# Kernel optimization log

Hardware: AMD Instinct MI355X
Metric: run time of the kernel (lower is better)

The kernel has to match this reference:

```python
import math
import jax, jax.numpy as jnp
import numpy as np

D_MODEL = 1024
N_HEAD = 16
HEAD_DIM = D_MODEL // N_HEAD


def _alibi_slopes(n_heads: int) -> np.ndarray:
    def pow2_slopes(n):
        start = 2.0 ** (-(2.0 ** (-(math.log2(n) - 3))))
        return [start * (start ** i) for i in range(n)]
    if math.log2(n_heads).is_integer():
        slopes = pow2_slopes(n_heads)
    else:
        cp2 = 2 ** math.floor(math.log2(n_heads))
        slopes = pow2_slopes(cp2)
        slopes += pow2_slopes(2 * cp2)[0::2][: n_heads - cp2]
    return np.asarray(slopes, dtype=np.float32)


def setup_inputs() -> dict:
    key = jax.random.key(0)
    ks = jax.random.split(key, 12)
    B, N, D = 2, 2048, D_MODEL
    s = 1.0 / math.sqrt(D)
    inp = {
        "x_q": jax.random.normal(ks[0], (B, N, D), dtype=jnp.float32),
        "x_kv": jax.random.normal(ks[1], (B, N, D), dtype=jnp.float32),
        "attn_bias": jax.random.normal(ks[2], (N, N), dtype=jnp.float32) * 0.1,
        "Wq": jax.random.normal(ks[3], (D, D), dtype=jnp.float32) * s,
        "bq": jnp.zeros((D,), dtype=jnp.float32),
        "Wk": jax.random.normal(ks[4], (D, D), dtype=jnp.float32) * s,
        "bk": jnp.zeros((D,), dtype=jnp.float32),
        "Wv": jax.random.normal(ks[5], (D, D), dtype=jnp.float32) * s,
        "bv": jnp.zeros((D,), dtype=jnp.float32),
        "Wo": jax.random.normal(ks[6], (D, D), dtype=jnp.float32) * s,
        "bo": jnp.zeros((D,), dtype=jnp.float32),
        "is_self_attn": 1,
        "causal": 1,
    }
    return inp


def reference(x_q, x_kv, attn_bias, Wq, bq, Wk, bk, Wv, bv, Wo, bo, is_self_attn, causal):
    B, Nq, D = x_q.shape
    Nk = x_kv.shape[1]
    H, hd = N_HEAD, HEAD_DIM

    # torch Linear: y = x @ W.T + b
    q = (jnp.einsum("bqd,ed->bqe", x_q, Wq) + bq).reshape(B, Nq, H, hd)
    k = (jnp.einsum("bkd,ed->bke", x_kv, Wk) + bk).reshape(B, Nk, H, hd)
    v = (jnp.einsum("bkd,ed->bke", x_kv, Wv) + bv).reshape(B, Nk, H, hd)

    logits = jnp.einsum("bqhd,bkhd->bhqk", q, k) / math.sqrt(hd)  # [B,H,Nq,Nk]

    if is_self_attn and Nq == Nk:
        i = jnp.arange(Nq)[:, None]
        j = jnp.arange(Nk)[None, :]
        dist = jnp.maximum(j - i, 0).astype(jnp.float32)  # [Nq,Nk]
        slopes = jnp.asarray(_alibi_slopes(H))  # [H]
        logits = logits - slopes[None, :, None, None] * dist[None, None]

    if attn_bias is not None:
        logits = logits + attn_bias[None, None]

    if causal and is_self_attn and Nq == Nk:
        mask = jnp.triu(jnp.ones((Nq, Nk), dtype=bool), k=1)
        logits = jnp.where(mask[None, None], -jnp.inf, logits)

    attn = jax.nn.softmax(logits, axis=-1)
    out = jnp.einsum("bhqk,bkhd->bqhd", attn, v).reshape(B, Nq, D)
    return jnp.einsum("bqd,ed->bqe", out, Wo) + bo
```

## Files before the change

### kernel.cpp

```cpp
#include <hip/hip_runtime.h>
#include <hip/hip_bf16.h>

typedef __attribute__((ext_vector_type(8))) short short8;
typedef __attribute__((ext_vector_type(4))) float floatx4;

#define NSEQ   2048
#define DMODEL 1024
#define NHEAD  16
#define HDIM   64
#define BATCH  2
#define LOG2E 1.44269504088896340736f

#define XF4   1048576u
#define WF4   262144u

__device__ __forceinline__ void gload16(const void* g, void* l) {
    __builtin_amdgcn_global_load_lds(
        (const __attribute__((address_space(1))) void*)g,
        (__attribute__((address_space(3))) void*)l, 16, 0, 0);
}

#define BARRIER() asm volatile("s_barrier" ::: "memory")
#define CFENCE()  asm volatile("" ::: "memory")

__device__ __forceinline__ float bf16lo(unsigned u) {
    union { unsigned i; float f; } c; c.i = u << 16; return c.f;
}
__device__ __forceinline__ float bf16hi(unsigned u) {
    union { unsigned i; float f; } c; c.i = u & 0xffff0000u; return c.f;
}

__global__ __launch_bounds__(256)
void cvt_all(const float* __restrict__ xq, const float* __restrict__ xkv,
             const float* __restrict__ wq, const float* __restrict__ wk,
             const float* __restrict__ wv, const float* __restrict__ wo,
             __hip_bfloat16* __restrict__ dxq, __hip_bfloat16* __restrict__ dxkv,
             __hip_bfloat16* __restrict__ dwq, __hip_bfloat16* __restrict__ dwk,
             __hip_bfloat16* __restrict__ dwv, __hip_bfloat16* __restrict__ dwo)
{
    const unsigned total = 2*XF4 + 4*WF4;
    const unsigned stride = gridDim.x * blockDim.x;
    for (unsigned i = blockIdx.x*blockDim.x + threadIdx.x; i < total; i += stride) {
        const float4* src; __hip_bfloat16* dst; unsigned off;
        if (i < XF4)        { src = (const float4*)xq;  dst = dxq;  off = i; }
        else if (i < 2*XF4) { src = (const float4*)xkv; dst = dxkv; off = i - XF4; }
        else {
            unsigned j = i - 2*XF4; unsigned ws = j >> 18; off = j & (WF4 - 1);
            src = (const float4*)(ws==0 ? wq : ws==1 ? wk : ws==2 ? wv : wo);
            dst = (ws==0 ? dwq : ws==1 ? dwk : ws==2 ? dwv : dwo);
        }
        float4 v = src[off];
        __hip_bfloat16 h[4] = {__float2bfloat16(v.x), __float2bfloat16(v.y),
                               __float2bfloat16(v.z), __float2bfloat16(v.w)};
        *reinterpret_cast<uint2*>(dst + (size_t)off*4) = *reinterpret_cast<uint2*>(h);
    }
}

__global__ __launch_bounds__(256)
void cvt_bias(const float* __restrict__ src, __hip_bfloat16* __restrict__ dst)
{
    const unsigned total = (unsigned)(NSEQ*(size_t)NSEQ/4);
    const unsigned stride = gridDim.x * blockDim.x;
    for (unsigned i = blockIdx.x*blockDim.x + threadIdx.x; i < total; i += stride) {
        float4 v = ((const float4*)src)[i];
        __hip_bfloat16 h[4] = {__float2bfloat16(v.x * LOG2E), __float2bfloat16(v.y * LOG2E),
                               __float2bfloat16(v.z * LOG2E), __float2bfloat16(v.w * LOG2E)};
        *reinterpret_cast<uint2*>(dst + (size_t)i*4) = *reinterpret_cast<uint2*>(h);
    }
}

struct QkvArgs {
    const __hip_bfloat16* A[3];
    const __hip_bfloat16* W[3];
    const float*          bias[3];
    __hip_bfloat16*       out[3];
};

__global__ __launch_bounds__(256)
void qkv_gemm(QkvArgs args)
{
    __shared__ __hip_bfloat16 S[256][72];

    const int tid  = threadIdx.x;
    const int lane = tid & 63;
    const int wv   = tid >> 6;
    const int wm   = wv >> 1, wn = wv & 1;
    const int l15  = lane & 15, l4 = lane >> 4;
    const int m0   = blockIdx.x * 128;
    const int n0   = blockIdx.y * 128;
    const int z    = blockIdx.z;

    const __hip_bfloat16* __restrict__ A = args.A[z];
    const __hip_bfloat16* __restrict__ W = args.W[z];

    floatx4 acc[4][4] = {};

    for (int k0 = 0; k0 < DMODEL; k0 += 64) {
        #pragma unroll
        for (int it = 0; it < 4; ++it) {
            const int sI   = tid + 256 * it;
            const int row  = sI >> 2;
            const int colq = (sI & 3) * 16;
            const __hip_bfloat16* src = (it < 2)
                ? A + (size_t)(m0 + row) * DMODEL + k0 + colq
                : W + (size_t)(n0 + row - 128) * DMODEL + k0 + colq;
            const uint4* s4 = reinterpret_cast<const uint4*>(src);
            *reinterpret_cast<uint4*>(&S[row][colq])     = s4[0];
            *reinterpret_cast<uint4*>(&S[row][colq + 8]) = s4[1];
        }
        __syncthreads();

        #pragma unroll
        for (int kk = 0; kk < 64; kk += 32) {
            short8 af[4], bf[4];
            #pragma unroll
            for (int mi = 0; mi < 4; ++mi)
                af[mi] = *reinterpret_cast<const short8*>(&S[wm*64 + mi*16 + l15][kk + l4*8]);
            #pragma unroll
            for (int nj = 0; nj < 4; ++nj)
                bf[nj] = *reinterpret_cast<const short8*>(&S[128 + wn*64 + nj*16 + l15][kk + l4*8]);
            #pragma unroll
            for (int mi = 0; mi < 4; ++mi)
                #pragma unroll
                for (int nj = 0; nj < 4; ++nj)
                    acc[mi][nj] = __builtin_amdgcn_mfma_f32_16x16x32_bf16(
                        af[mi], bf[nj], acc[mi][nj], 0, 0, 0);
        }
        __syncthreads();
    }

    const float* bias = args.bias[z];
    __hip_bfloat16* C = args.out[z];
    const bool vt = (z == 2);
    #pragma unroll
    for (int mi = 0; mi < 4; ++mi) {
        const int mbase = m0 + wm*64 + mi*16 + l4*4;
        #pragma unroll
        for (int nj = 0; nj < 4; ++nj) {
            const int nn = n0 + wn*64 + nj*16 + l15;
            const float bb = bias[nn];
            const int h = nn >> 6, d = nn & (HDIM - 1);
            #pragma unroll
            for (int r = 0; r < 4; ++r) {
                const int m = mbase + r;
                const int b = m >> 11, n = m & (NSEQ - 1);
                const float val = acc[mi][nj][r] + bb;
                if (!vt)
                    C[((size_t)(b*NHEAD + h) * NSEQ + n) * HDIM + d] = __float2bfloat16(val);
                else
                    C[((size_t)(b*NHEAD + h) * HDIM + d) * NSEQ + n] = __float2bfloat16(val);
            }
        }
    }
}

__global__ __launch_bounds__(256)
void oproj_gemm(const __hip_bfloat16* __restrict__ A, const __hip_bfloat16* __restrict__ W,
                const float* __restrict__ bias, float* __restrict__ C)
{
    __shared__ __hip_bfloat16 S[192][72];

    const int tid  = threadIdx.x;
    const int lane = tid & 63;
    const int wv   = tid >> 6;
    const int l15  = lane & 15, l4 = lane >> 4;
    const int m0   = blockIdx.x * 64;
    const int n0   = blockIdx.y * 128;

    floatx4 acc[4][2] = {};

    for (int k0 = 0; k0 < DMODEL; k0 += 64) {
        #pragma unroll
        for (int it = 0; it < 3; ++it) {
            const int sI   = tid + 256 * it;
            const int row  = sI >> 2;
            const int colq = (sI & 3) * 16;
            const __hip_bfloat16* src = (it < 1)
                ? A + (size_t)(m0 + row) * DMODEL + k0 + colq
                : W + (size_t)(n0 + row - 64) * DMODEL + k0 + colq;
            const uint4* s4 = reinterpret_cast<const uint4*>(src);
            *reinterpret_cast<uint4*>(&S[row][colq])     = s4[0];
            *reinterpret_cast<uint4*>(&S[row][colq + 8]) = s4[1];
        }
        __syncthreads();

        #pragma unroll
        for (int kk = 0; kk < 64; kk += 32) {
            short8 af[4], bf[2];
            #pragma unroll
            for (int mi = 0; mi < 4; ++mi)
                af[mi] = *reinterpret_cast<const short8*>(&S[mi*16 + l15][kk + l4*8]);
            #pragma unroll
            for (int nj = 0; nj < 2; ++nj)
                bf[nj] = *reinterpret_cast<const short8*>(&S[64 + wv*32 + nj*16 + l15][kk + l4*8]);
            #pragma unroll
            for (int mi = 0; mi < 4; ++mi)
                #pragma unroll
                for (int nj = 0; nj < 2; ++nj)
                    acc[mi][nj] = __builtin_amdgcn_mfma_f32_16x16x32_bf16(
                        af[mi], bf[nj], acc[mi][nj], 0, 0, 0);
        }
        __syncthreads();
    }

    #pragma unroll
    for (int mi = 0; mi < 4; ++mi) {
        const int mbase = m0 + mi*16 + l4*4;
        #pragma unroll
        for (int nj = 0; nj < 2; ++nj) {
            const int nn = n0 + wv*32 + nj*16 + l15;
            const float bb = bias[nn];
            #pragma unroll
            for (int r = 0; r < 4; ++r)
                C[(size_t)(mbase + r) * DMODEL + nn] = acc[mi][nj][r] + bb;
        }
    }
}

__global__ __launch_bounds__(256)
void flash_attn(const __hip_bfloat16* __restrict__ Q,
                const __hip_bfloat16* __restrict__ K,
                const __hip_bfloat16* __restrict__ VT,
                const __hip_bfloat16* __restrict__ Bb,
                const int* __restrict__ selfp,
                const int* __restrict__ causalp,
                __hip_bfloat16* __restrict__ Oout)
{
    __shared__ __align__(16) char KB[2][8192];
    __shared__ __align__(16) char VB[2][8192];
    __shared__ __align__(16) char BBUF[2][8192];
    __shared__ __align__(16) char PL[4][2048];

    const int tid  = threadIdx.x;
    const int lane = tid & 63;
    const int wv   = tid >> 6;
    const int l15  = lane & 15, l4 = lane >> 4;

    const int g   = blockIdx.x;
    const int bh  = g & 31;
    const int u   = g >> 5;
    const int qA  = u, qB = 31 - u;
    const int h   = bh & (NHEAD - 1);
    const int b   = bh >> 4;

    const int selfF   = selfp[0];
    const int causalF = causalp[0];
    const bool cz      = (selfF != 0) && (causalF != 0);
    const bool alibiOn = (selfF != 0) && (causalF == 0);
    const float slopeL2 = exp2f(-(8.0f / NHEAD) * (float)(h + 1)) * LOG2E;

    const char* Kh = (const char*)(K  + (size_t)bh * NSEQ * HDIM);
    const char* Vh = (const char*)(VT + (size_t)bh * HDIM * NSEQ);
    const __hip_bfloat16* Qh = Q + (size_t)bh * NSEQ * HDIM;

    const int nA = cz ? (qA + 1) : (NSEQ/64);
    const int NT = cz ? 33 : (NSEQ/32);

    const int qa0 = qA*64 + wv*16, qb0 = qB*64 + wv*16;
    const short8 qfA0 = *(const short8*)&Qh[(qa0 + l15)*HDIM + l4*8];
    const short8 qfA1 = *(const short8*)&Qh[(qa0 + l15)*HDIM + 32 + l4*8];
    const short8 qfB0 = *(const short8*)&Qh[(qb0 + l15)*HDIM + l4*8];
    const short8 qfB1 = *(const short8*)&Qh[(qb0 + l15)*HDIM + 32 + l4*8];
    CFENCE();

    const int srow = lane >> 3;
    const int co   = (((lane & 7) ^ srow) << 4);

    auto stage = [&](int it_, int bi) {
        int qq, jt;
        if (it_ < nA) { qq = qA; jt = it_; } else { qq = qB; jt = it_ - nA; }
        const int j0 = jt << 6;
        const char* Bh = (const char*)Bb + (size_t)qq * 64 * (NSEQ*2);
        #pragma unroll
        for (int i2 = 0; i2 < 2; ++i2) {
            const int rl = wv*16 + i2*8 + srow;
            const int db = (wv*16 + i2*8) * 128;
            gload16(Kh + (size_t)(j0 + rl)*128 + co,          &KB[bi][db]);
            gload16(Vh + (size_t)rl*4096 + (size_t)j0*2 + co, &VB[bi][db]);
            gload16(Bh + (size_t)rl*4096 + (size_t)j0*2 + co, &BBUF[bi][db]);
        }
    };

    char* plw = &PL[wv][l15 * 128];
    const int swq = (l15 & 7) << 4;
    const int rowb = wv*16 + l15;
    const int swb  = (rowb & 7) << 4;

    floatx4 o[4] = {};
    float lr = 0.f;
    short8 qf0 = qfA0, qf1 = qfA1;
    int qbc = qA;

    stage(0, 0);
    int cur = 0;
    for (int it = 0; it < NT; ++it) {
        if (it + 1 < NT) {
            stage(it + 1, cur ^ 1);
            asm volatile("s_waitcnt vmcnt(6)" ::: "memory");
        } else {
            asm volatile("s_waitcnt vmcnt(0)" ::: "memory");
        }
        BARRIER();

        const char* kb = KB[cur];
        const char* vb = VB[cur];
        const char* bb = BBUF[cur];

        floatx4 s4[4];
        __builtin_amdgcn_s_setprio(1);
        #pragma unroll
        for (int tt = 0; tt < 4; ++tt) {
            const int row = tt*16 + l15;
            const int sw  = (row & 7) << 4;
            const short8 kf0 = *(const short8*)(kb + ((row*128 + l4*16)      ^ sw));
            const short8 kf1 = *(const short8*)(kb + ((row*128 + 64 + l4*16) ^ sw));
            floatx4 z = {};
            z      = __builtin_amdgcn_mfma_f32_16x16x32_bf16(kf0, qf0, z, 0, 0, 0);
            s4[tt] = __builtin_amdgcn_mfma_f32_16x16x32_bf16(kf1, qf1, z, 0, 0, 0);
        }
        __builtin_amdgcn_s_setprio(0);

        uint2 bl[4];
        #pragma unroll
        for (int tt = 0; tt < 4; ++tt)
            bl[tt] = *(const uint2*)(bb + ((rowb*128 + tt*32 + l4*8) ^ swb));

        const bool domask = cz && (it == nA - 1 || it == NT - 1);
        const int qloc = wv*16 + l15;
        #pragma unroll
        for (int tt = 0; tt < 4; ++tt) {
            float bf[4];
            bf[0] = bf16lo(bl[tt].x); bf[1] = bf16hi(bl[tt].x);
            bf[2] = bf16lo(bl[tt].y); bf[3] = bf16hi(bl[tt].y);
            float e[4];
            #pragma unroll
            for (int r = 0; r < 4; ++r) {
                const int jloc = tt*16 + l4*4 + r;
                float v2 = fmaf(s4[tt][r], 0.125f * LOG2E, bf[r]);
                if (alibiOn) {
                    const int jg = ((it < nA) ? it : it - nA)*64 + jloc;
                    const int dd = jg - (qbc*64 + qloc);
                    if (dd > 0) v2 = fmaf((float)dd, -slopeL2, v2);
                }
                e[r] = __builtin_amdgcn_exp2f(v2);
                if (domask && jloc > qloc) e[r] = 0.0f;
                lr += e[r];
            }
            unsigned p0, p1;
            asm("v_cvt_pk_bf16_f32 %0, %1, %2" : "=v"(p0) : "v"(e[0]), "v"(e[1]));
            asm("v_cvt_pk_bf16_f32 %0, %1, %2" : "=v"(p1) : "v"(e[2]), "v"(e[3]));
            uint2 pw; pw.x = p0; pw.y = p1;
            *(uint2*)(plw + ((tt*32 + l4*8) ^ swq)) = pw;
        }

        const short8 pf0 = *(const short8*)(plw + ((l4*16)      ^ swq));
        const short8 pf1 = *(const short8*)(plw + ((64 + l4*16) ^ swq));

        __builtin_amdgcn_s_setprio(1);
        #pragma unroll
        for (int dt = 0; dt < 4; ++dt) {
            const int row = dt*16 + l15;
            const int sw  = (row & 7) << 4;
            const short8 vf0 = *(const short8*)(vb + ((row*128 + l4*16)      ^ sw));
            const short8 vf1 = *(const short8*)(vb + ((row*128 + 64 + l4*16) ^ sw));
            o[dt] = __builtin_amdgcn_mfma_f32_16x16x32_bf16(pf0, vf0, o[dt], 0, 0, 0);
            o[dt] = __builtin_amdgcn_mfma_f32_16x16x32_bf16(pf1, vf1, o[dt], 0, 0, 0);
        }
        __builtin_amdgcn_s_setprio(0);

        BARRIER();
        cur ^= 1;

        if (it == nA - 1 || it == NT - 1) {
            float t = lr;
            t += __shfl_xor(t, 16);
            t += __shfl_xor(t, 32);
            #pragma unroll
            for (int r = 0; r < 4; ++r) {
                const float lq  = __shfl(t, l4*4 + r);
                const float inv = 1.0f / lq;
                const int n = qbc*64 + wv*16 + l4*4 + r;
                #pragma unroll
                for (int dt = 0; dt < 4; ++dt)
                    Oout[((size_t)(b*NSEQ + n)) * DMODEL + h*HDIM + dt*16 + l15] =
                        __float2bfloat16(o[dt][r] * inv);
            }
            if (it == nA - 1) {
                #pragma unroll
                for (int dt = 0; dt < 4; ++dt) o[dt] = floatx4{0.f, 0.f, 0.f, 0.f};
                lr = 0.f;
                qf0 = qfB0; qf1 = qfB1; qbc = qB;
            }
        }
    }
}

extern "C" void kernel_launch(void* const* d_in, const int* in_sizes, int n_in,
                              void* d_out, int out_size, void* d_ws, size_t ws_size,
                              hipStream_t stream)
{
    (void)in_sizes; (void)n_in; (void)out_size; (void)ws_size;
    const float* x_q  = (const float*)d_in[0];
    const float* x_kv = (const float*)d_in[1];
    const float* ab   = (const float*)d_in[2];
    const float* Wq   = (const float*)d_in[3];
    const float* bq   = (const float*)d_in[4];
    const float* Wk   = (const float*)d_in[5];
    const float* bk   = (const float*)d_in[6];
    const float* Wv   = (const float*)d_in[7];
    const float* bv   = (const float*)d_in[8];
    const float* Wo   = (const float*)d_in[9];
    const float* bo   = (const float*)d_in[10];
    const int* selfp   = (const int*)d_in[11];
    const int* causalp = (const int*)d_in[12];

    const size_t XB = (size_t)BATCH * NSEQ * DMODEL * sizeof(__hip_bfloat16);
    const size_t WB = (size_t)DMODEL * DMODEL * sizeof(__hip_bfloat16);
    char* ws = (char*)d_ws;
    __hip_bfloat16* xq_b  = (__hip_bfloat16*)(ws);
    __hip_bfloat16* AO    = (__hip_bfloat16*)(ws);
    __hip_bfloat16* xkv_b = (__hip_bfloat16*)(ws + XB);
    __hip_bfloat16* ab_b  = (__hip_bfloat16*)(ws + XB);
    __hip_bfloat16* Wq_b  = (__hip_bfloat16*)(ws + 2*XB);
    __hip_bfloat16* Wk_b  = (__hip_bfloat16*)(ws + 2*XB + WB);
    __hip_bfloat16* Wv_b  = (__hip_bfloat16*)(ws + 2*XB + 2*WB);
    __hip_bfloat16* Wo_b  = (__hip_bfloat16*)(ws + 2*XB + 3*WB);
    __hip_bfloat16* Qb    = (__hip_bfloat16*)(ws + 2*XB + 4*WB);
    __hip_bfloat16* Kb    = (__hip_bfloat16*)(ws + 2*XB + 4*WB + XB);
    __hip_bfloat16* VTb   = (__hip_bfloat16*)(ws + 2*XB + 4*WB + 2*XB);

    cvt_all<<<dim3(2048), dim3(256), 0, stream>>>(
        x_q, x_kv, Wq, Wk, Wv, Wo, xq_b, xkv_b, Wq_b, Wk_b, Wv_b, Wo_b);

    QkvArgs qa;
    qa.A[0] = xq_b;  qa.A[1] = xkv_b; qa.A[2] = xkv_b;
    qa.W[0] = Wq_b;  qa.W[1] = Wk_b;  qa.W[2] = Wv_b;
    qa.bias[0] = bq; qa.bias[1] = bk; qa.bias[2] = bv;
    qa.out[0] = Qb;  qa.out[1] = Kb;  qa.out[2] = VTb;
    qkv_gemm<<<dim3(32, 8, 3), dim3(256), 0, stream>>>(qa);

    cvt_bias<<<dim3(1024), dim3(256), 0, stream>>>(ab, ab_b);

    flash_attn<<<dim3(512), dim3(256), 0, stream>>>(
        Qb, Kb, VTb, ab_b, selfp, causalp, AO);

    oproj_gemm<<<dim3(64, 8), dim3(256), 0, stream>>>(AO, Wo_b, bo, (float*)d_out);
}
```

Before: 132.9 us.

## Split flash attention query tile and key range across waves, double grid

The flash attention kernel now launches twice as many blocks, each handling half of a 64-row query tile. The four waves are arranged as two query groups times two key halves, and the partial outputs and row sums are merged through shared memory at the end of each tile. V fragments are now loaded directly from global memory into registers rather than staged in LDS, which shrinks LDS use and allows a 4-blocks-per-CU launch bound. The aim is more occupancy and parallelism, at the cost of duplicated K loads per block, extra barriers for the merge, and uncached-through-LDS V reads.

```diff
diff --git a/kernel.cpp b/kernel.cpp
--- a/kernel.cpp
+++ b/kernel.cpp
@@ -217,7 +217,7 @@
     }
 }
 
-__global__ __launch_bounds__(256)
+__global__ __launch_bounds__(256, 4)
 void flash_attn(const __hip_bfloat16* __restrict__ Q,
                 const __hip_bfloat16* __restrict__ K,
                 const __hip_bfloat16* __restrict__ VT,
@@ -227,18 +227,23 @@
                 __hip_bfloat16* __restrict__ Oout)
 {
     __shared__ __align__(16) char KB[2][8192];
-    __shared__ __align__(16) char VB[2][8192];
-    __shared__ __align__(16) char BBUF[2][8192];
-    __shared__ __align__(16) char PL[4][2048];
+    __shared__ __align__(16) char BBUF[2][4096];
+    __shared__ __hip_bfloat16 PL[4][16][40];
+    __shared__ float OX[2][16][68];
+    __shared__ float LR[2][16];
 
     const int tid  = threadIdx.x;
     const int lane = tid & 63;
     const int wv   = tid >> 6;
     const int l15  = lane & 15, l4 = lane >> 4;
+    const int qg   = wv >> 1;
+    const int jh   = wv & 1;
 
     const int g   = blockIdx.x;
     const int bh  = g & 31;
-    const int u   = g >> 5;
+    const int rem = g >> 5;
+    const int u   = rem & 15;
+    const int rh  = rem >> 4;
     const int qA  = u, qB = 31 - u;
     const int h   = bh & (NHEAD - 1);
     const int b   = bh >> 4;
@@ -254,13 +259,14 @@
     const __hip_bfloat16* Qh = Q + (size_t)bh * NSEQ * HDIM;
 
     const int nA = cz ? (qA + 1) : (NSEQ/64);
-    const int NT = cz ? 33 : (NSEQ/32);
-
-    const int qa0 = qA*64 + wv*16, qb0 = qB*64 + wv*16;
-    const short8 qfA0 = *(const short8*)&Qh[(qa0 + l15)*HDIM + l4*8];
-    const short8 qfA1 = *(const short8*)&Qh[(qa0 + l15)*HDIM + 32 + l4*8];
-    const short8 qfB0 = *(const short8*)&Qh[(qb0 + l15)*HDIM + l4*8];
-    const short8 qfB1 = *(const short8*)&Qh[(qb0 + l15)*HDIM + 32 + l4*8];
+    const int NT = cz ? 33 : (2*NSEQ/64);
+
+    const int qloc = rh*32 + qg*16 + l15;
+
+    const short8 qfA0 = *(const short8*)&Qh[(qA*64 + qloc)*HDIM + l4*8];
+    const short8 qfA1 = *(const short8*)&Qh[(qA*64 + qloc)*HDIM + 32 + l4*8];
+    const short8 qfB0 = *(const short8*)&Qh[(qB*64 + qloc)*HDIM + l4*8];
+    const short8 qfB1 = *(const short8*)&Qh[(qB*64 + qloc)*HDIM + 32 + l4*8];
     CFENCE();
 
     const int srow = lane >> 3;
@@ -270,47 +276,51 @@
         int qq, jt;
         if (it_ < nA) { qq = qA; jt = it_; } else { qq = qB; jt = it_ - nA; }
         const int j0 = jt << 6;
-        const char* Bh = (const char*)Bb + (size_t)qq * 64 * (NSEQ*2);
         #pragma unroll
         for (int i2 = 0; i2 < 2; ++i2) {
             const int rl = wv*16 + i2*8 + srow;
-            const int db = (wv*16 + i2*8) * 128;
-            gload16(Kh + (size_t)(j0 + rl)*128 + co,          &KB[bi][db]);
-            gload16(Vh + (size_t)rl*4096 + (size_t)j0*2 + co, &VB[bi][db]);
-            gload16(Bh + (size_t)rl*4096 + (size_t)j0*2 + co, &BBUF[bi][db]);
-        }
+            gload16(Kh + (size_t)(j0 + rl)*128 + co, &KB[bi][(wv*16 + i2*8) * 128]);
+        }
+        const int rb = qq*64 + rh*32 + wv*8 + srow;
+        gload16((const char*)Bb + (size_t)rb*4096 + (size_t)j0*2 + co,
+                &BBUF[bi][wv*8*128]);
     };
 
-    char* plw = &PL[wv][l15 * 128];
-    const int swq = (l15 & 7) << 4;
-    const int rowb = wv*16 + l15;
-    const int swb  = (rowb & 7) << 4;
+    char* plw = (char*)&PL[wv][0][0] + l15*80;
 
     floatx4 o[4] = {};
     float lr = 0.f;
     short8 qf0 = qfA0, qf1 = qfA1;
-    int qbc = qA;
+    int qtile = qA;
 
     stage(0, 0);
     int cur = 0;
     for (int it = 0; it < NT; ++it) {
+        const int jt = (it < nA) ? it : it - nA;
+
+        short8 vf[4];
+        const int jv = (jt*64 + jh*32) * 2;
+        #pragma unroll
+        for (int dt = 0; dt < 4; ++dt)
+            vf[dt] = *(const short8*)(Vh + (size_t)(dt*16 + l15)*4096 + jv + l4*16);
+        CFENCE();
+
         if (it + 1 < NT) {
             stage(it + 1, cur ^ 1);
-            asm volatile("s_waitcnt vmcnt(6)" ::: "memory");
+            asm volatile("s_waitcnt vmcnt(7)" ::: "memory");
         } else {
-            asm volatile("s_waitcnt vmcnt(0)" ::: "memory");
+            asm volatile("s_waitcnt vmcnt(4)" ::: "memory");
         }
         BARRIER();
 
         const char* kb = KB[cur];
-        const char* vb = VB[cur];
-        const char* bb = BBUF[cur];
-
-        floatx4 s4[4];
+        const char* bbuf = BBUF[cur];
+
+        floatx4 s4[2];
         __builtin_amdgcn_s_setprio(1);
         #pragma unroll
-        for (int tt = 0; tt < 4; ++tt) {
-            const int row = tt*16 + l15;
+        for (int tt = 0; tt < 2; ++tt) {
+            const int row = jh*32 + tt*16 + l15;
             const int sw  = (row & 7) << 4;
             const short8 kf0 = *(const short8*)(kb + ((row*128 + l4*16)      ^ sw));
             const short8 kf1 = *(const short8*)(kb + ((row*128 + 64 + l4*16) ^ sw));
@@ -320,26 +330,26 @@
         }
         __builtin_amdgcn_s_setprio(0);
 
-        uint2 bl[4];
-        #pragma unroll
-        for (int tt = 0; tt < 4; ++tt)
-            bl[tt] = *(const uint2*)(bb + ((rowb*128 + tt*32 + l4*8) ^ swb));
+        const int rowb = qg*16 + l15;
+        const int swb  = (rowb & 7) << 4;
+        uint2 bl[2];
+        #pragma unroll
+        for (int tt = 0; tt < 2; ++tt)
+            bl[tt] = *(const uint2*)(bbuf + ((rowb*128 + jh*64 + tt*32 + l4*8) ^ swb));
 
         const bool domask = cz && (it == nA - 1 || it == NT - 1);
-        const int qloc = wv*16 + l15;
-        #pragma unroll
-        for (int tt = 0; tt < 4; ++tt) {
+        #pragma unroll
+        for (int tt = 0; tt < 2; ++tt) {
             float bf[4];
             bf[0] = bf16lo(bl[tt].x); bf[1] = bf16hi(bl[tt].x);
             bf[2] = bf16lo(bl[tt].y); bf[3] = bf16hi(bl[tt].y);
             float e[4];
             #pragma unroll
             for (int r = 0; r < 4; ++r) {
-                const int jloc = tt*16 + l4*4 + r;
+                const int jloc = jh*32 + tt*16 + l4*4 + r;
                 float v2 = fmaf(s4[tt][r], 0.125f * LOG2E, bf[r]);
                 if (alibiOn) {
-                    const int jg = ((it < nA) ? it : it - nA)*64 + jloc;
-                    const int dd = jg - (qbc*64 + qloc);
+                    const int dd = (jt*64 + jloc) - (qtile*64 + qloc);
                     if (dd > 0) v2 = fmaf((float)dd, -slopeL2, v2);
                 }
                 e[r] = __builtin_amdgcn_exp2f(v2);
@@ -350,22 +360,15 @@
             asm("v_cvt_pk_bf16_f32 %0, %1, %2" : "=v"(p0) : "v"(e[0]), "v"(e[1]));
             asm("v_cvt_pk_bf16_f32 %0, %1, %2" : "=v"(p1) : "v"(e[2]), "v"(e[3]));
             uint2 pw; pw.x = p0; pw.y = p1;
-            *(uint2*)(plw + ((tt*32 + l4*8) ^ swq)) = pw;
-        }
-
-        const short8 pf0 = *(const short8*)(plw + ((l4*16)      ^ swq));
-        const short8 pf1 = *(const short8*)(plw + ((64 + l4*16) ^ swq));
+            *(uint2*)(plw + tt*32 + l4*8) = pw;
+        }
+
+        const short8 pf = *(const short8*)(plw + l4*16);
 
         __builtin_amdgcn_s_setprio(1);
         #pragma unroll
-        for (int dt = 0; dt < 4; ++dt) {
-            const int row = dt*16 + l15;
-            const int sw  = (row & 7) << 4;
-            const short8 vf0 = *(const short8*)(vb + ((row*128 + l4*16)      ^ sw));
-            const short8 vf1 = *(const short8*)(vb + ((row*128 + 64 + l4*16) ^ sw));
-            o[dt] = __builtin_amdgcn_mfma_f32_16x16x32_bf16(pf0, vf0, o[dt], 0, 0, 0);
-            o[dt] = __builtin_amdgcn_mfma_f32_16x16x32_bf16(pf1, vf1, o[dt], 0, 0, 0);
-        }
+        for (int dt = 0; dt < 4; ++dt)
+            o[dt] = __builtin_amdgcn_mfma_f32_16x16x32_bf16(pf, vf[dt], o[dt], 0, 0, 0);
         __builtin_amdgcn_s_setprio(0);
 
         BARRIER();
@@ -375,21 +378,36 @@
             float t = lr;
             t += __shfl_xor(t, 16);
             t += __shfl_xor(t, 32);
-            #pragma unroll
-            for (int r = 0; r < 4; ++r) {
-                const float lq  = __shfl(t, l4*4 + r);
-                const float inv = 1.0f / lq;
-                const int n = qbc*64 + wv*16 + l4*4 + r;
+            if (jh == 1) {
                 #pragma unroll
                 for (int dt = 0; dt < 4; ++dt)
-                    Oout[((size_t)(b*NSEQ + n)) * DMODEL + h*HDIM + dt*16 + l15] =
-                        __float2bfloat16(o[dt][r] * inv);
+                    #pragma unroll
+                    for (int r = 0; r < 4; ++r)
+                        OX[qg][l4*4 + r][dt*16 + l15] = o[dt][r];
+                if (lane < 16) LR[qg][l15] = t;
             }
+            __syncthreads();
+            if (jh == 0) {
+                const float lt = t + LR[qg][l15];
+                #pragma unroll
+                for (int r = 0; r < 4; ++r) {
+                    const float lq  = __shfl(lt, l4*4 + r);
+                    const float inv = 1.0f / lq;
+                    const int n = qtile*64 + rh*32 + qg*16 + l4*4 + r;
+                    #pragma unroll
+                    for (int dt = 0; dt < 4; ++dt) {
+                        const float val = (o[dt][r] + OX[qg][l4*4 + r][dt*16 + l15]) * inv;
+                        Oout[((size_t)(b*NSEQ + n)) * DMODEL + h*HDIM + dt*16 + l15] =
+                            __float2bfloat16(val);
+                    }
+                }
+            }
+            __syncthreads();
             if (it == nA - 1) {
                 #pragma unroll
                 for (int dt = 0; dt < 4; ++dt) o[dt] = floatx4{0.f, 0.f, 0.f, 0.f};
                 lr = 0.f;
-                qf0 = qfB0; qf1 = qfB1; qbc = qB;
+                qf0 = qfB0; qf1 = qfB1; qtile = qB;
             }
         }
     }
@@ -441,7 +459,7 @@
 
     cvt_bias<<<dim3(1024), dim3(256), 0, stream>>>(ab, ab_b);
 
-    flash_attn<<<dim3(512), dim3(256), 0, stream>>>(
+    flash_attn<<<dim3(1024), dim3(256), 0, stream>>>(
         Qb, Kb, VTb, ab_b, selfp, causalp, AO);
 
     oproj_gemm<<<dim3(64, 8), dim3(256), 0, stream>>>(AO, Wo_b, bo, (float*)d_out);
```

Result: slower. 158.9 us (+19.6%).

## Process two adjacent query tiles per block sharing K/V loads in flash attention

Applied to the files above, without the earlier changes.

Each attention block now handles a contiguous 128-row query strip as two 64-row tiles, instead of a balanced pair of far-apart 64-row tiles. Both tiles consume the same staged K and V fragments, which halves K/V global traffic per query row. It also means a single causal mask check and a single epilogue per tile. In exchange, per-block work becomes uneven (2 to 32 iterations), which is only partly mitigated by interleaving the heavy and light strips in block order. Shared memory also grows, for a doubled bias buffer and P scratch, and launch bounds now request 2 blocks per CU.

```diff
diff --git a/kernel.cpp b/kernel.cpp
--- a/kernel.cpp
+++ b/kernel.cpp
@@ -217,7 +217,7 @@
     }
 }
 
-__global__ __launch_bounds__(256)
+__global__ __launch_bounds__(256, 2)
 void flash_attn(const __hip_bfloat16* __restrict__ Q,
                 const __hip_bfloat16* __restrict__ K,
                 const __hip_bfloat16* __restrict__ VT,
@@ -228,8 +228,8 @@
 {
     __shared__ __align__(16) char KB[2][8192];
     __shared__ __align__(16) char VB[2][8192];
-    __shared__ __align__(16) char BBUF[2][8192];
-    __shared__ __align__(16) char PL[4][2048];
+    __shared__ __align__(16) char BBUF[2][16384];
+    __shared__ __align__(16) char PL[4][4096];
 
     const int tid  = threadIdx.x;
     const int lane = tid & 63;
@@ -238,8 +238,8 @@
 
     const int g   = blockIdx.x;
     const int bh  = g & 31;
-    const int u   = g >> 5;
-    const int qA  = u, qB = 31 - u;
+    const int ip  = g >> 5;
+    const int t   = (ip < 8) ? ip : 23 - ip;
     const int h   = bh & (NHEAD - 1);
     const int b   = bh >> 4;
 
@@ -253,50 +253,56 @@
     const char* Vh = (const char*)(VT + (size_t)bh * HDIM * NSEQ);
     const __hip_bfloat16* Qh = Q + (size_t)bh * NSEQ * HDIM;
 
-    const int nA = cz ? (qA + 1) : (NSEQ/64);
-    const int NT = cz ? 33 : (NSEQ/32);
-
-    const int qa0 = qA*64 + wv*16, qb0 = qB*64 + wv*16;
-    const short8 qfA0 = *(const short8*)&Qh[(qa0 + l15)*HDIM + l4*8];
-    const short8 qfA1 = *(const short8*)&Qh[(qa0 + l15)*HDIM + 32 + l4*8];
-    const short8 qfB0 = *(const short8*)&Qh[(qb0 + l15)*HDIM + l4*8];
-    const short8 qfB1 = *(const short8*)&Qh[(qb0 + l15)*HDIM + 32 + l4*8];
+    const int NT = cz ? (2*t + 2) : (NSEQ/64);
+
+    const int q0g = t*128 + wv*16;
+    const int q1g = q0g + 64;
+    const short8 qf00 = *(const short8*)&Qh[(q0g + l15)*HDIM + l4*8];
+    const short8 qf01 = *(const short8*)&Qh[(q0g + l15)*HDIM + 32 + l4*8];
+    const short8 qf10 = *(const short8*)&Qh[(q1g + l15)*HDIM + l4*8];
+    const short8 qf11 = *(const short8*)&Qh[(q1g + l15)*HDIM + 32 + l4*8];
     CFENCE();
 
     const int srow = lane >> 3;
     const int co   = (((lane & 7) ^ srow) << 4);
 
-    auto stage = [&](int it_, int bi) {
-        int qq, jt;
-        if (it_ < nA) { qq = qA; jt = it_; } else { qq = qB; jt = it_ - nA; }
+    const char* Bh = (const char*)Bb + (size_t)(t*128) * (NSEQ*2);
+
+    auto stage = [&](int jt, int bi) {
         const int j0 = jt << 6;
-        const char* Bh = (const char*)Bb + (size_t)qq * 64 * (NSEQ*2);
         #pragma unroll
         for (int i2 = 0; i2 < 2; ++i2) {
             const int rl = wv*16 + i2*8 + srow;
             const int db = (wv*16 + i2*8) * 128;
             gload16(Kh + (size_t)(j0 + rl)*128 + co,          &KB[bi][db]);
             gload16(Vh + (size_t)rl*4096 + (size_t)j0*2 + co, &VB[bi][db]);
-            gload16(Bh + (size_t)rl*4096 + (size_t)j0*2 + co, &BBUF[bi][db]);
+        }
+        #pragma unroll
+        for (int i2 = 0; i2 < 4; ++i2) {
+            const int rb = wv*32 + i2*8 + srow;
+            const int db = (wv*32 + i2*8) * 128;
+            gload16(Bh + (size_t)rb*4096 + (size_t)j0*2 + co, &BBUF[bi][db]);
         }
     };
 
-    char* plw = &PL[wv][l15 * 128];
+    char* plw0 = &PL[wv][l15 * 128];
+    char* plw1 = &PL[wv][2048 + l15 * 128];
     const int swq = (l15 & 7) << 4;
-    const int rowb = wv*16 + l15;
-    const int swb  = (rowb & 7) << 4;
-
-    floatx4 o[4] = {};
-    float lr = 0.f;
-    short8 qf0 = qfA0, qf1 = qfA1;
-    int qbc = qA;
+    const int rowb0 = wv*16 + l15;
+    const int rowb1 = 64 + wv*16 + l15;
+    const int swb0 = (rowb0 & 7) << 4;
+    const int swb1 = (rowb1 & 7) << 4;
+
+    floatx4 o0[4] = {}, o1[4] = {};
+    float lr0 = 0.f, lr1 = 0.f;
 
     stage(0, 0);
+    CFENCE();
     int cur = 0;
-    for (int it = 0; it < NT; ++it) {
-        if (it + 1 < NT) {
-            stage(it + 1, cur ^ 1);
-            asm volatile("s_waitcnt vmcnt(6)" ::: "memory");
+    for (int jt = 0; jt < NT; ++jt) {
+        if (jt + 1 < NT) {
+            stage(jt + 1, cur ^ 1);
+            asm volatile("s_waitcnt vmcnt(8)" ::: "memory");
         } else {
             asm volatile("s_waitcnt vmcnt(0)" ::: "memory");
         }
@@ -306,91 +312,156 @@
         const char* vb = VB[cur];
         const char* bb = BBUF[cur];
 
-        floatx4 s4[4];
-        __builtin_amdgcn_s_setprio(1);
+        const bool g0act = !cz || (jt <= 2*t);
+
+        short8 kf0[4], kf1[4];
         #pragma unroll
         for (int tt = 0; tt < 4; ++tt) {
             const int row = tt*16 + l15;
             const int sw  = (row & 7) << 4;
-            const short8 kf0 = *(const short8*)(kb + ((row*128 + l4*16)      ^ sw));
-            const short8 kf1 = *(const short8*)(kb + ((row*128 + 64 + l4*16) ^ sw));
+            kf0[tt] = *(const short8*)(kb + ((row*128 + l4*16)      ^ sw));
+            kf1[tt] = *(const short8*)(kb + ((row*128 + 64 + l4*16) ^ sw));
+        }
+
+        floatx4 s40[4], s41[4];
+        __builtin_amdgcn_s_setprio(1);
+        if (g0act) {
+            #pragma unroll
+            for (int tt = 0; tt < 4; ++tt) {
+                floatx4 z = {};
+                z       = __builtin_amdgcn_mfma_f32_16x16x32_bf16(kf0[tt], qf00, z, 0, 0, 0);
+                s40[tt] = __builtin_amdgcn_mfma_f32_16x16x32_bf16(kf1[tt], qf01, z, 0, 0, 0);
+            }
+        }
+        #pragma unroll
+        for (int tt = 0; tt < 4; ++tt) {
             floatx4 z = {};
-            z      = __builtin_amdgcn_mfma_f32_16x16x32_bf16(kf0, qf0, z, 0, 0, 0);
-            s4[tt] = __builtin_amdgcn_mfma_f32_16x16x32_bf16(kf1, qf1, z, 0, 0, 0);
+            z       = __builtin_amdgcn_mfma_f32_16x16x32_bf16(kf0[tt], qf10, z, 0, 0, 0);
+            s41[tt] = __builtin_amdgcn_mfma_f32_16x16x32_bf16(kf1[tt], qf11, z, 0, 0, 0);
         }
         __builtin_amdgcn_s_setprio(0);
 
-        uint2 bl[4];
-        #pragma unroll
-        for (int tt = 0; tt < 4; ++tt)
-            bl[tt] = *(const uint2*)(bb + ((rowb*128 + tt*32 + l4*8) ^ swb));
-
-        const bool domask = cz && (it == nA - 1 || it == NT - 1);
-        const int qloc = wv*16 + l15;
-        #pragma unroll
-        for (int tt = 0; tt < 4; ++tt) {
-            float bf[4];
-            bf[0] = bf16lo(bl[tt].x); bf[1] = bf16hi(bl[tt].x);
-            bf[2] = bf16lo(bl[tt].y); bf[3] = bf16hi(bl[tt].y);
-            float e[4];
-            #pragma unroll
-            for (int r = 0; r < 4; ++r) {
-                const int jloc = tt*16 + l4*4 + r;
-                float v2 = fmaf(s4[tt][r], 0.125f * LOG2E, bf[r]);
-                if (alibiOn) {
-                    const int jg = ((it < nA) ? it : it - nA)*64 + jloc;
-                    const int dd = jg - (qbc*64 + qloc);
-                    if (dd > 0) v2 = fmaf((float)dd, -slopeL2, v2);
-                }
-                e[r] = __builtin_amdgcn_exp2f(v2);
-                if (domask && jloc > qloc) e[r] = 0.0f;
-                lr += e[r];
-            }
-            unsigned p0, p1;
-            asm("v_cvt_pk_bf16_f32 %0, %1, %2" : "=v"(p0) : "v"(e[0]), "v"(e[1]));
-            asm("v_cvt_pk_bf16_f32 %0, %1, %2" : "=v"(p1) : "v"(e[2]), "v"(e[3]));
-            uint2 pw; pw.x = p0; pw.y = p1;
-            *(uint2*)(plw + ((tt*32 + l4*8) ^ swq)) = pw;
-        }
-
-        const short8 pf0 = *(const short8*)(plw + ((l4*16)      ^ swq));
-        const short8 pf1 = *(const short8*)(plw + ((64 + l4*16) ^ swq));
-
-        __builtin_amdgcn_s_setprio(1);
+        short8 vfA[4], vfB[4];
         #pragma unroll
         for (int dt = 0; dt < 4; ++dt) {
             const int row = dt*16 + l15;
             const int sw  = (row & 7) << 4;
-            const short8 vf0 = *(const short8*)(vb + ((row*128 + l4*16)      ^ sw));
-            const short8 vf1 = *(const short8*)(vb + ((row*128 + 64 + l4*16) ^ sw));
-            o[dt] = __builtin_amdgcn_mfma_f32_16x16x32_bf16(pf0, vf0, o[dt], 0, 0, 0);
-            o[dt] = __builtin_amdgcn_mfma_f32_16x16x32_bf16(pf1, vf1, o[dt], 0, 0, 0);
-        }
-        __builtin_amdgcn_s_setprio(0);
+            vfA[dt] = *(const short8*)(vb + ((row*128 + l4*16)      ^ sw));
+            vfB[dt] = *(const short8*)(vb + ((row*128 + 64 + l4*16) ^ sw));
+        }
+
+        if (g0act) {
+            uint2 bl[4];
+            #pragma unroll
+            for (int tt = 0; tt < 4; ++tt)
+                bl[tt] = *(const uint2*)(bb + ((rowb0*128 + tt*32 + l4*8) ^ swb0));
+            const bool domask = cz && (jt == 2*t);
+            #pragma unroll
+            for (int tt = 0; tt < 4; ++tt) {
+                float bf[4];
+                bf[0] = bf16lo(bl[tt].x); bf[1] = bf16hi(bl[tt].x);
+                bf[2] = bf16lo(bl[tt].y); bf[3] = bf16hi(bl[tt].y);
+                float e[4];
+                #pragma unroll
+                for (int r = 0; r < 4; ++r) {
+                    const int jloc = tt*16 + l4*4 + r;
+                    float v2 = fmaf(s40[tt][r], 0.125f * LOG2E, bf[r]);
+                    if (alibiOn) {
+                        const int dd = (jt*64 + jloc) - (q0g + l15);
+                        if (dd > 0) v2 = fmaf((float)dd, -slopeL2, v2);
+                    }
+                    e[r] = __builtin_amdgcn_exp2f(v2);
+                    if (domask && jloc > (wv*16 + l15)) e[r] = 0.0f;
+                    lr0 += e[r];
+                }
+                unsigned p0, p1;
+                asm("v_cvt_pk_bf16_f32 %0, %1, %2" : "=v"(p0) : "v"(e[0]), "v"(e[1]));
+                asm("v_cvt_pk_bf16_f32 %0, %1, %2" : "=v"(p1) : "v"(e[2]), "v"(e[3]));
+                uint2 pw; pw.x = p0; pw.y = p1;
+                *(uint2*)(plw0 + ((tt*32 + l4*8) ^ swq)) = pw;
+            }
+            const short8 pf0 = *(const short8*)(plw0 + ((l4*16)      ^ swq));
+            const short8 pf1 = *(const short8*)(plw0 + ((64 + l4*16) ^ swq));
+            __builtin_amdgcn_s_setprio(1);
+            #pragma unroll
+            for (int dt = 0; dt < 4; ++dt) {
+                o0[dt] = __builtin_amdgcn_mfma_f32_16x16x32_bf16(pf0, vfA[dt], o0[dt], 0, 0, 0);
+                o0[dt] = __builtin_amdgcn_mfma_f32_16x16x32_bf16(pf1, vfB[dt], o0[dt], 0, 0, 0);
+            }
+            __builtin_amdgcn_s_setprio(0);
+        }
+
+        {
+            uint2 bl[4];
+            #pragma unroll
+            for (int tt = 0; tt < 4; ++tt)
+                bl[tt] = *(const uint2*)(bb + ((rowb1*128 + tt*32 + l4*8) ^ swb1));
+            const bool domask = cz && (jt == NT - 1);
+            #pragma unroll
+            for (int tt = 0; tt < 4; ++tt) {
+                float bf[4];
+                bf[0] = bf16lo(bl[tt].x); bf[1] = bf16hi(bl[tt].x);
+                bf[2] = bf16lo(bl[tt].y); bf[3] = bf16hi(bl[tt].y);
+                float e[4];
+                #pragma unroll
+                for (int r = 0; r < 4; ++r) {
+                    const int jloc = tt*16 + l4*4 + r;
+                    float v2 = fmaf(s41[tt][r], 0.125f * LOG2E, bf[r]);
+                    if (alibiOn) {
+                        const int dd = (jt*64 + jloc) - (q1g + l15);
+                        if (dd > 0) v2 = fmaf((float)dd, -slopeL2, v2);
+                    }
+                    e[r] = __builtin_amdgcn_exp2f(v2);
+                    if (domask && jloc > (wv*16 + l15)) e[r] = 0.0f;
+                    lr1 += e[r];
+                }
+                unsigned p0, p1;
+                asm("v_cvt_pk_bf16_f32 %0, %1, %2" : "=v"(p0) : "v"(e[0]), "v"(e[1]));
+                asm("v_cvt_pk_bf16_f32 %0, %1, %2" : "=v"(p1) : "v"(e[2]), "v"(e[3]));
+                uint2 pw; pw.x = p0; pw.y = p1;
+                *(uint2*)(plw1 + ((tt*32 + l4*8) ^ swq)) = pw;
+            }
+            const short8 pf0 = *(const short8*)(plw1 + ((l4*16)      ^ swq));
+            const short8 pf1 = *(const short8*)(plw1 + ((64 + l4*16) ^ swq));
+            __builtin_amdgcn_s_setprio(1);
+            #pragma unroll
+            for (int dt = 0; dt < 4; ++dt) {
+                o1[dt] = __builtin_amdgcn_mfma_f32_16x16x32_bf16(pf0, vfA[dt], o1[dt], 0, 0, 0);
+                o1[dt] = __builtin_amdgcn_mfma_f32_16x16x32_bf16(pf1, vfB[dt], o1[dt], 0, 0, 0);
+            }
+            __builtin_amdgcn_s_setprio(0);
+        }
 
         BARRIER();
         cur ^= 1;
-
-        if (it == nA - 1 || it == NT - 1) {
-            float t = lr;
-            t += __shfl_xor(t, 16);
-            t += __shfl_xor(t, 32);
-            #pragma unroll
-            for (int r = 0; r < 4; ++r) {
-                const float lq  = __shfl(t, l4*4 + r);
-                const float inv = 1.0f / lq;
-                const int n = qbc*64 + wv*16 + l4*4 + r;
-                #pragma unroll
-                for (int dt = 0; dt < 4; ++dt)
-                    Oout[((size_t)(b*NSEQ + n)) * DMODEL + h*HDIM + dt*16 + l15] =
-                        __float2bfloat16(o[dt][r] * inv);
-            }
-            if (it == nA - 1) {
-                #pragma unroll
-                for (int dt = 0; dt < 4; ++dt) o[dt] = floatx4{0.f, 0.f, 0.f, 0.f};
-                lr = 0.f;
-                qf0 = qfB0; qf1 = qfB1; qbc = qB;
-            }
+    }
+
+    {
+        float tt0 = lr0;
+        tt0 += __shfl_xor(tt0, 16);
+        tt0 += __shfl_xor(tt0, 32);
+        #pragma unroll
+        for (int r = 0; r < 4; ++r) {
+            const float lq  = __shfl(tt0, l4*4 + r);
+            const float inv = 1.0f / lq;
+            const int n = t*128 + wv*16 + l4*4 + r;
+            #pragma unroll
+            for (int dt = 0; dt < 4; ++dt)
+                Oout[((size_t)(b*NSEQ + n)) * DMODEL + h*HDIM + dt*16 + l15] =
+                    __float2bfloat16(o0[dt][r] * inv);
+        }
+        float tt1 = lr1;
+        tt1 += __shfl_xor(tt1, 16);
+        tt1 += __shfl_xor(tt1, 32);
+        #pragma unroll
+        for (int r = 0; r < 4; ++r) {
+            const float lq  = __shfl(tt1, l4*4 + r);
+            const float inv = 1.0f / lq;
+            const int n = t*128 + 64 + wv*16 + l4*4 + r;
+            #pragma unroll
+            for (int dt = 0; dt < 4; ++dt)
+                Oout[((size_t)(b*NSEQ + n)) * DMODEL + h*HDIM + dt*16 + l15] =
+                    __float2bfloat16(o1[dt][r] * inv);
         }
     }
 }
```

Measured after the change: 142.1 us. +6.9%, slower.
